# Kernel optimization log

Hardware: AMD Instinct MI355X
Metric: run time of the kernel (lower is better)

Reference implementation:

```python
import jax, jax.numpy as jnp
import numpy as np

D_MODEL = 1024
HEADS = 16
D_KEY = D_MODEL // HEADS


def setup_inputs() -> dict:
    key = jax.random.key(0)
    ks = jax.random.split(key, 7)
    B, S = 4, 2048
    queries = jax.random.normal(ks[0], (B, S, D_MODEL), dtype=jnp.float32)
    keys = jax.random.normal(ks[1], (B, S, D_MODEL), dtype=jnp.float32)
    values = jax.random.normal(ks[2], (B, S, D_MODEL), dtype=jnp.float32)
    scale = 1.0 / np.sqrt(D_MODEL)
    # Per-head projection weights, torch Linear layout [out=d_key, in=d_model], stacked over heads
    Wq = jax.random.uniform(ks[3], (HEADS, D_KEY, D_MODEL), jnp.float32, -scale, scale)
    Wk = jax.random.uniform(ks[4], (HEADS, D_KEY, D_MODEL), jnp.float32, -scale, scale)
    Wv = jax.random.uniform(ks[5], (HEADS, D_KEY, D_MODEL), jnp.float32, -scale, scale)
    Wo = jax.random.uniform(ks[6], (D_MODEL, D_MODEL), jnp.float32, -scale, scale)
    return {"queries": queries, "keys": keys, "values": values,
            "Wq": Wq, "Wk": Wk, "Wv": Wv, "Wo": Wo}


def reference(queries, keys, values, Wq, Wk, Wv, Wo):
    # Project per head: [B,S,D] x [H,K,D] -> [B,H,S,K]
    q = jnp.einsum('bsd,hkd->bhsk', queries, Wq)
    k = jnp.einsum('bsd,hkd->bhsk', keys, Wk)
    v = jnp.einsum('bsd,hkd->bhsk', values, Wv)
    attn = jnp.einsum('bhqk,bhsk->bhqs', q, k) / jnp.sqrt(jnp.float32(D_KEY))
    attn = jax.nn.softmax(attn, axis=-1)
    out = jnp.einsum('bhqs,bhsk->bhqk', attn, v)  # [B,H,S,K]
    B, H, S, K = out.shape
    # concat heads along last dim (head order = torch cat order)
    out = out.transpose(0, 2, 1, 3).reshape(B, S, H * K)
    return out @ Wo.T
```

## Files before the change

kernel.cpp:

```cpp
#include <hip/hip_runtime.h>
#include <hip/hip_bf16.h>

typedef __attribute__((ext_vector_type(8))) short short8;
typedef __attribute__((ext_vector_type(4))) short short4v;
typedef __attribute__((ext_vector_type(4))) float f32x4;
typedef __bf16 bf16x8 __attribute__((ext_vector_type(8)));
typedef __attribute__((ext_vector_type(2))) unsigned int u32x2;
typedef __attribute__((ext_vector_type(4))) unsigned int u32x4;

#define DEVI static __device__ __forceinline__

DEVI short f2bs(float f) {
    union { __hip_bfloat16 h; short s; } u;
    u.h = __float2bfloat16(f);
    return u.s;
}

DEVI unsigned pack2(float a, float b) {
    union { short s[2]; unsigned u; } u;
    u.s[0] = f2bs(a);
    u.s[1] = f2bs(b);
    return u.u;
}

DEVI void xchg(unsigned& x, unsigned& y) {
#if __has_builtin(__builtin_amdgcn_permlane32_swap) && __has_builtin(__builtin_amdgcn_permlane16_swap)
    u32x2 t = __builtin_amdgcn_permlane32_swap(x, y, false, false);
    u32x2 r = __builtin_amdgcn_permlane16_swap(t[0], t[1], false, false);
    x = r[0];
    y = r[1];
#else
    asm("v_permlane32_swap_b32 %0, %1" : "+v"(x), "+v"(y));
    asm("v_permlane16_swap_b32 %0, %1" : "+v"(x), "+v"(y));
#endif
}

DEVI f32x4 mfma16(short8 a, short8 b, f32x4 c) {
    return __builtin_amdgcn_mfma_f32_16x16x32_bf16(
        __builtin_bit_cast(bf16x8, a), __builtin_bit_cast(bf16x8, b), c, 0, 0, 0);
}

DEVI void glds16(const short* g, short* l) {
    __builtin_amdgcn_global_load_lds((const __attribute__((address_space(1))) void*)g,
                                     (__attribute__((address_space(3))) void*)l, 16, 0, 0);
}

__global__ __launch_bounds__(256) void cvt_all(const float4* __restrict__ q,
                                               const float4* __restrict__ k,
                                               const float4* __restrict__ v,
                                               const float4* __restrict__ wq,
                                               const float4* __restrict__ wk,
                                               const float4* __restrict__ wv,
                                               const float4* __restrict__ wo,
                                               short4v* __restrict__ dq,
                                               short4v* __restrict__ dk,
                                               short4v* __restrict__ dv,
                                               short4v* __restrict__ dwq,
                                               short4v* __restrict__ dwk,
                                               short4v* __restrict__ dwv,
                                               short4v* __restrict__ dwo) {
    int bid = blockIdx.x;
    float4 x;
    short4v s;
    if (bid < 8192) {
        int i = bid * 256 + threadIdx.x;
        x = q[i]; s.x = f2bs(x.x); s.y = f2bs(x.y); s.z = f2bs(x.z); s.w = f2bs(x.w); dq[i] = s;
        x = k[i]; s.x = f2bs(x.x); s.y = f2bs(x.y); s.z = f2bs(x.z); s.w = f2bs(x.w); dk[i] = s;
        x = v[i]; s.x = f2bs(x.x); s.y = f2bs(x.y); s.z = f2bs(x.z); s.w = f2bs(x.w); dv[i] = s;
    } else {
        int i = (bid - 8192) * 256 + threadIdx.x;
        x = wq[i]; s.x = f2bs(x.x); s.y = f2bs(x.y); s.z = f2bs(x.z); s.w = f2bs(x.w); dwq[i] = s;
        x = wk[i]; s.x = f2bs(x.x); s.y = f2bs(x.y); s.z = f2bs(x.z); s.w = f2bs(x.w); dwk[i] = s;
        x = wv[i]; s.x = f2bs(x.x); s.y = f2bs(x.y); s.z = f2bs(x.z); s.w = f2bs(x.w); dwv[i] = s;
        x = wo[i]; s.x = f2bs(x.x); s.y = f2bs(x.y); s.z = f2bs(x.z); s.w = f2bs(x.w); dwo[i] = s;
    }
}

template <typename EpiT>
DEVI void gemm_body(const short* A, const short* Bw, short* smem, int m0, int n0, EpiT epi) {
    const int t = threadIdx.x;
    const int lane = t & 63, w = t >> 6;
    const int col = lane & 15, quad = lane >> 4;
    const int wm = (w & 1) * 64, wn = (w >> 1) * 64;

    const short* pA0;
    const short* pA1;
    const short* pB0;
    const short* pB1;
    {
        int i0 = w * 64 + lane, i1 = (4 + w) * 64 + lane;
        int L0 = i0 >> 3, cc0 = (i0 & 7) ^ (L0 & 7);
        int r0 = 2 * L0 + (cc0 & 1), c0 = cc0 >> 1;
        int L1 = i1 >> 3, cc1 = (i1 & 7) ^ (L1 & 7);
        int r1 = 2 * L1 + (cc1 & 1), c1 = cc1 >> 1;
        pA0 = A + (size_t)(m0 + r0) * 1024 + c0 * 8;
        pA1 = A + (size_t)(m0 + r1) * 1024 + c1 * 8;
        pB0 = Bw + (size_t)(n0 + r0) * 1024 + c0 * 8;
        pB1 = Bw + (size_t)(n0 + r1) * 1024 + c1 * 8;
    }
    const int posa = (2 * quad + (col & 1)) ^ (col >> 1);
    const int base_a = wm * 32 + (col >> 1) * 64 + posa * 8;
    const int base_b = wn * 32 + (col >> 1) * 64 + posa * 8;

    f32x4 acc[4][4];
#pragma unroll
    for (int i = 0; i < 4; ++i)
#pragma unroll
        for (int j = 0; j < 4; ++j) acc[i][j] = (f32x4){0.f, 0.f, 0.f, 0.f};

    glds16(pA0, smem + w * 512);
    glds16(pA1, smem + (4 + w) * 512);
    glds16(pB0, smem + 4096 + w * 512);
    glds16(pB1, smem + 4096 + (4 + w) * 512);
    pA0 += 32; pA1 += 32; pB0 += 32; pB1 += 32;
    __syncthreads();

#pragma unroll 2
    for (int kt = 0; kt < 32; ++kt) {
        const int cur = kt & 1;
        const short* Cb = smem + cur * 8192;
        if (kt < 31) {
            short* Nb = smem + (cur ^ 1) * 8192;
            glds16(pA0, Nb + w * 512);
            glds16(pA1, Nb + (4 + w) * 512);
            glds16(pB0, Nb + 4096 + w * 512);
            glds16(pB1, Nb + 4096 + (4 + w) * 512);
            pA0 += 32; pA1 += 32; pB0 += 32; pB1 += 32;
        }
        short8 a[4], b[4];
#pragma unroll
        for (int i = 0; i < 4; ++i) a[i] = *(const short8*)(Cb + base_a + i * 512);
#pragma unroll
        for (int i = 0; i < 4; ++i) b[i] = *(const short8*)(Cb + 4096 + base_b + i * 512);
        __builtin_amdgcn_s_setprio(1);
#pragma unroll
        for (int mi = 0; mi < 4; ++mi)
#pragma unroll
            for (int ni = 0; ni < 4; ++ni)
                acc[mi][ni] = mfma16(a[mi], b[ni], acc[mi][ni]);
        __builtin_amdgcn_s_setprio(0);
        __syncthreads();
    }
    epi(acc, wm, wn, col, quad);
}

__global__ __launch_bounds__(256) void qkv_gemm(const short* __restrict__ xq,
                                                const short* __restrict__ xk,
                                                const short* __restrict__ xv,
                                                const short* __restrict__ wq,
                                                const short* __restrict__ wk,
                                                const short* __restrict__ wv,
                                                short* __restrict__ qp,
                                                short* __restrict__ kp,
                                                short* __restrict__ vpt, float qscale) {
    __shared__ __align__(16) short smem[17408];
    const int lin = blockIdx.x + (blockIdx.y << 3) + (blockIdx.z << 9);
    const int wgid = (lin & 7) * 192 + (lin >> 3);
    const int n0 = (wgid & 7) * 128;
    const int m0 = ((wgid >> 3) & 63) * 128;
    const int z = wgid >> 9;
    const short* A = (z == 0) ? xq : (z == 1) ? xk : xv;
    const short* W = (z == 0) ? wq : (z == 1) ? wk : wv;

    if (z < 2) {
        short* outs = (z == 0) ? qp : kp;
        const float scale = (z == 0) ? qscale : 1.0f;
        gemm_body(A, W, smem, m0, n0, [&](f32x4 (&acc)[4][4], int wm, int wn, int col, int quad) {
            short* T = smem;
#pragma unroll
            for (int mi = 0; mi < 4; ++mi)
#pragma unroll
                for (int ni = 0; ni < 4; ++ni)
#pragma unroll
                    for (int r = 0; r < 4; ++r)
                        T[(wm + mi * 16 + quad * 4 + r) * 136 + wn + ni * 16 + col] =
                            f2bs(acc[mi][ni][r] * scale);
            __syncthreads();
            int t = threadIdx.x;
            int ml = t >> 1, nh = (t & 1) * 64;
            int m = m0 + ml;
            int b = m >> 11, s = m & 2047;
#pragma unroll
            for (int j = 0; j < 8; ++j) {
                int n = n0 + nh + j * 8;
                short8 vv = *(const short8*)(T + ml * 136 + nh + j * 8);
                size_t off = ((size_t)(b * 16 + (n >> 6)) * 2048 + s) * 64 + (n & 63);
                *(short8*)(outs + off) = vv;
            }
        });
    } else {
        gemm_body(A, W, smem, m0, n0, [&](f32x4 (&acc)[4][4], int wm, int wn, int col, int quad) {
            short* T = smem;
#pragma unroll
            for (int mi = 0; mi < 4; ++mi)
#pragma unroll
                for (int ni = 0; ni < 4; ++ni) {
                    int n_l = wn + ni * 16 + col;
                    int m_l = wm + mi * 16 + quad * 4;
                    short4v sv;
                    sv.x = f2bs(acc[mi][ni][0]); sv.y = f2bs(acc[mi][ni][1]);
                    sv.z = f2bs(acc[mi][ni][2]); sv.w = f2bs(acc[mi][ni][3]);
                    *(short4v*)(T + n_l * 132 + m_l) = sv;
                }
            __syncthreads();
            int t = threadIdx.x;
            int nrow = t >> 1, mh = (t & 1) * 64;
            int b = m0 >> 11, s0 = m0 & 2047;
            size_t base = ((size_t)(b * 1024 + n0 + nrow)) * 2048 + s0 + mh;
#pragma unroll
            for (int j = 0; j < 16; ++j) {
                unsigned long long vv = *(const unsigned long long*)(T + nrow * 132 + mh + j * 4);
                *(unsigned long long*)(vpt + base + j * 4) = vv;
            }
        });
    }
}

__global__ __launch_bounds__(256) void out_gemm(const short* __restrict__ ao,
                                                const short* __restrict__ wo,
                                                float* __restrict__ outf) {
    __shared__ __align__(16) short smem[16896];
    const int lin = blockIdx.x + (blockIdx.y << 3);
    const int wgid = (lin & 7) * 64 + (lin >> 3);
    const int n0 = (wgid & 7) * 128;
    const int m0 = (wgid >> 3) * 128;
    gemm_body(ao, wo, smem, m0, n0, [&](f32x4 (&acc)[4][4], int wm, int wn, int col, int quad) {
#pragma unroll
        for (int mi = 0; mi < 4; ++mi)
#pragma unroll
            for (int ni = 0; ni < 4; ++ni)
#pragma unroll
                for (int r = 0; r < 4; ++r) {
                    int m = m0 + wm + mi * 16 + quad * 4 + r;
                    int n = n0 + wn + ni * 16 + col;
                    outf[(size_t)m * 1024 + n] = acc[mi][ni][r];
                }
    });
}

__global__ __launch_bounds__(256, 4) void flash_attn(const short* __restrict__ qp,
                                                     const short* __restrict__ kp,
                                                     const short* __restrict__ vpt,
                                                     short* __restrict__ ao) {
    __shared__ __align__(16) short smem[16384];
    short* Ks2 = smem;
    short* Vs2 = smem + 8192;

    const int t = threadIdx.x, lane = t & 63, w = t >> 6;
    const int col = lane & 15, quad = lane >> 4;
    const int bh = blockIdx.x, q0 = blockIdx.y * 128;
    const short* qb = qp + (size_t)bh * 2048 * 64;
    const short* kb = kp + (size_t)bh * 2048 * 64;
    const short* vb = vpt + (size_t)bh * 64 * 2048;

#pragma unroll
    for (int j = 0; j < 4; ++j) {
        int cbase = (j * 4 + w) * 64;
        int c = cbase + lane;
        int row = c >> 3, kc = (c & 7) ^ (row & 7);
        glds16(qb + (size_t)(q0 + row) * 64 + kc * 8, smem + cbase * 8);
    }
    __syncthreads();
    short8 bQ[2][2];
#pragma unroll
    for (int qi = 0; qi < 2; ++qi)
#pragma unroll
        for (int ks = 0; ks < 2; ++ks) {
            int row = w * 32 + qi * 16 + col;
            int kc = (ks * 4 + quad) ^ (col & 7);
            bQ[qi][ks] = *(const short8*)(smem + (row * 8 + kc) * 8);
        }
    __syncthreads();

    const int base2_0 = col * 64 + ((quad ^ (col & 7)) * 8);
    const int base2_1 = col * 64 + (((4 + quad) ^ (col & 7)) * 8);

    const short* kg0;
    const short* kg1;
    const short* vg0;
    const short* vg1;
    {
        int c0 = w * 64 + lane, c1 = (4 + w) * 64 + lane;
        int r0 = c0 >> 3, p0 = c0 & 7, r1 = c1 >> 3, p1 = c1 & 7;
        kg0 = kb + r0 * 64 + ((p0 ^ (r0 & 7)) * 8);
        kg1 = kb + r1 * 64 + ((p1 ^ (r1 & 7)) * 8);
        vg0 = vb + (size_t)r0 * 2048 + ((p0 ^ (r0 & 7)) * 8);
        vg1 = vb + (size_t)r1 * 2048 + ((p1 ^ (r1 & 7)) * 8);
    }

    f32x4 acc_o[2][4], acc_l[2];
#pragma unroll
    for (int qi = 0; qi < 2; ++qi) {
        acc_l[qi] = (f32x4){0.f, 0.f, 0.f, 0.f};
#pragma unroll
        for (int ni = 0; ni < 4; ++ni) acc_o[qi][ni] = (f32x4){0.f, 0.f, 0.f, 0.f};
    }
    const short ONE = 0x3F80;
    const short8 vones = {ONE, ONE, ONE, ONE, ONE, ONE, ONE, ONE};

    glds16(kg0, Ks2 + w * 512);
    glds16(kg1, Ks2 + (4 + w) * 512);
    glds16(vg0, Vs2 + w * 512);
    glds16(vg1, Vs2 + (4 + w) * 512);
    kg0 += 4096; kg1 += 4096; vg0 += 64; vg1 += 64;
    __syncthreads();

#pragma unroll 2
    for (int kt = 0; kt < 32; ++kt) {
        const int cur = kt & 1;
        if (kt < 31) {
            const int nxt = cur ^ 1;
            glds16(kg0, Ks2 + nxt * 4096 + w * 512);
            glds16(kg1, Ks2 + nxt * 4096 + (4 + w) * 512);
            glds16(vg0, Vs2 + nxt * 4096 + w * 512);
            glds16(vg1, Vs2 + nxt * 4096 + (4 + w) * 512);
            kg0 += 4096; kg1 += 4096; vg0 += 64; vg1 += 64;
        }
        const short* Ks = Ks2 + cur * 4096;
        const short* Vs = Vs2 + cur * 4096;

#pragma unroll
        for (int g = 0; g < 2; ++g) {
            unsigned pdw[2][4];
#pragma unroll
            for (int h = 0; h < 2; ++h) {
                const int kei = g * 2 + h;
                f32x4 st0 = (f32x4){0.f, 0.f, 0.f, 0.f};
                f32x4 st1 = (f32x4){0.f, 0.f, 0.f, 0.f};
                __builtin_amdgcn_s_setprio(1);
                {
                    short8 aK0 = *(const short8*)(Ks + base2_0 + kei * 1024);
                    st0 = mfma16(aK0, bQ[0][0], st0);
                    st1 = mfma16(aK0, bQ[1][0], st1);
                    short8 aK1 = *(const short8*)(Ks + base2_1 + kei * 1024);
                    st0 = mfma16(aK1, bQ[0][1], st0);
                    st1 = mfma16(aK1, bQ[1][1], st1);
                }
                __builtin_amdgcn_s_setprio(0);
                {
                    float p0 = __builtin_amdgcn_exp2f(st0[0]);
                    float p1 = __builtin_amdgcn_exp2f(st0[1]);
                    float p2 = __builtin_amdgcn_exp2f(st0[2]);
                    float p3 = __builtin_amdgcn_exp2f(st0[3]);
                    pdw[0][h * 2] = pack2(p0, p1);
                    pdw[0][h * 2 + 1] = pack2(p2, p3);
                }
                {
                    float p0 = __builtin_amdgcn_exp2f(st1[0]);
                    float p1 = __builtin_amdgcn_exp2f(st1[1]);
                    float p2 = __builtin_amdgcn_exp2f(st1[2]);
                    float p3 = __builtin_amdgcn_exp2f(st1[3]);
                    pdw[1][h * 2] = pack2(p0, p1);
                    pdw[1][h * 2 + 1] = pack2(p2, p3);
                }
            }
            xchg(pdw[0][0], pdw[0][2]);
            xchg(pdw[0][1], pdw[0][3]);
            xchg(pdw[1][0], pdw[1][2]);
            xchg(pdw[1][1], pdw[1][3]);
            u32x4 pv0 = {pdw[0][0], pdw[0][1], pdw[0][2], pdw[0][3]};
            u32x4 pv1 = {pdw[1][0], pdw[1][1], pdw[1][2], pdw[1][3]};
            short8 pa0 = __builtin_bit_cast(short8, pv0);
            short8 pa1 = __builtin_bit_cast(short8, pv1);

            const int vb2 = (g == 0) ? base2_0 : base2_1;
            __builtin_amdgcn_s_setprio(1);
#pragma unroll
            for (int ni = 0; ni < 4; ++ni) {
                short8 bv = *(const short8*)(Vs + vb2 + ni * 1024);
                acc_o[0][ni] = mfma16(pa0, bv, acc_o[0][ni]);
                acc_o[1][ni] = mfma16(pa1, bv, acc_o[1][ni]);
            }
            acc_l[0] = mfma16(pa0, vones, acc_l[0]);
            acc_l[1] = mfma16(pa1, vones, acc_l[1]);
            __builtin_amdgcn_s_setprio(0);
        }
        __syncthreads();
    }

    const int b = bh >> 4, hd = bh & 15;
#pragma unroll
    for (int qi = 0; qi < 2; ++qi)
#pragma unroll
        for (int r = 0; r < 4; ++r) {
            float inv = 1.0f / acc_l[qi][r];
            int q = q0 + w * 32 + qi * 16 + quad * 4 + r;
#pragma unroll
            for (int ni = 0; ni < 4; ++ni)
                ao[((size_t)(b * 2048 + q)) * 1024 + hd * 64 + ni * 16 + col] =
                    f2bs(acc_o[qi][ni][r] * inv);
        }
}

extern "C" void kernel_launch(void* const* d_in, const int* in_sizes, int n_in,
                              void* d_out, int out_size, void* d_ws, size_t ws_size,
                              hipStream_t stream) {
    const float* q  = (const float*)d_in[0];
    const float* k  = (const float*)d_in[1];
    const float* v  = (const float*)d_in[2];
    const float* Wq = (const float*)d_in[3];
    const float* Wk = (const float*)d_in[4];
    const float* Wv = (const float*)d_in[5];
    const float* Wo = (const float*)d_in[6];
    float* out = (float*)d_out;

    short* ws = (short*)d_ws;
    const size_t SZ = (size_t)64 * 2048 * 64;
    const size_t WZ = (size_t)1024 * 1024;
    short* xq  = ws;
    short* xk  = ws + SZ;
    short* xv  = ws + 2 * SZ;
    short* qp  = ws + 3 * SZ;
    short* kp  = ws + 4 * SZ;
    short* wqb = ws + 5 * SZ;
    short* wkb = wqb + WZ;
    short* wvb = wqb + 2 * WZ;
    short* wob = wqb + 3 * WZ;
    short* ao  = xq;
    short* vpt = (short*)d_out;

    const float QSCALE = 0.125f * 1.44269504088896f;

    cvt_all<<<dim3(9216), dim3(256), 0, stream>>>(
        (const float4*)q, (const float4*)k, (const float4*)v, (const float4*)Wq,
        (const float4*)Wk, (const float4*)Wv, (const float4*)Wo, (short4v*)xq, (short4v*)xk,
        (short4v*)xv, (short4v*)wqb, (short4v*)wkb, (short4v*)wvb, (short4v*)wob);
    dim3 blk(256);
    qkv_gemm<<<dim3(8, 64, 3), blk, 0, stream>>>(xq, xk, xv, wqb, wkb, wvb, qp, kp, vpt, QSCALE);
    flash_attn<<<dim3(64, 16), blk, 0, stream>>>(qp, kp, vpt, ao);
    out_gemm<<<dim3(8, 64), blk, 0, stream>>>(ao, wob, out);
}
```

Measured before the change: 331.0 us.

## Switch flash attention inner loop to 32x32x16 bf16 MFMA tiles

Rewrites the attention kernel's QK^T and PV products to use 32x32x16 MFMA instead of 16x16x32, with each wave owning a 32-row Q tile. The P fragment shuffle drops to a single permlane32 swap and the row-sum accumulator becomes one 16-wide tile. The aim is fewer MFMA issues, fewer LDS fragment reads and fewer lane permutes per key tile. In exchange it changes the register layout and exp/pack scheduling, with some risk to register pressure and occupancy at four waves per SIMD.

```diff
diff --git a/kernel.cpp b/kernel.cpp
--- a/kernel.cpp
+++ b/kernel.cpp
@@ -4,6 +4,7 @@
 typedef __attribute__((ext_vector_type(8))) short short8;
 typedef __attribute__((ext_vector_type(4))) short short4v;
 typedef __attribute__((ext_vector_type(4))) float f32x4;
+typedef __attribute__((ext_vector_type(16))) float f32x16;
 typedef __bf16 bf16x8 __attribute__((ext_vector_type(8)));
 typedef __attribute__((ext_vector_type(2))) unsigned int u32x2;
 typedef __attribute__((ext_vector_type(4))) unsigned int u32x4;
@@ -23,20 +24,17 @@
     return u.u;
 }
 
-DEVI void xchg(unsigned& x, unsigned& y) {
-#if __has_builtin(__builtin_amdgcn_permlane32_swap) && __has_builtin(__builtin_amdgcn_permlane16_swap)
-    u32x2 t = __builtin_amdgcn_permlane32_swap(x, y, false, false);
-    u32x2 r = __builtin_amdgcn_permlane16_swap(t[0], t[1], false, false);
-    x = r[0];
-    y = r[1];
-#else
-    asm("v_permlane32_swap_b32 %0, %1" : "+v"(x), "+v"(y));
-    asm("v_permlane16_swap_b32 %0, %1" : "+v"(x), "+v"(y));
-#endif
+DEVI u32x2 pl32(unsigned x, unsigned y) {
+    return __builtin_amdgcn_permlane32_swap(x, y, false, false);
 }
 
 DEVI f32x4 mfma16(short8 a, short8 b, f32x4 c) {
     return __builtin_amdgcn_mfma_f32_16x16x32_bf16(
+        __builtin_bit_cast(bf16x8, a), __builtin_bit_cast(bf16x8, b), c, 0, 0, 0);
+}
+
+DEVI f32x16 mfma32(short8 a, short8 b, f32x16 c) {
+    return __builtin_amdgcn_mfma_f32_32x32x16_bf16(
         __builtin_bit_cast(bf16x8, a), __builtin_bit_cast(bf16x8, b), c, 0, 0, 0);
 }
 
@@ -247,7 +245,7 @@
     short* Vs2 = smem + 8192;
 
     const int t = threadIdx.x, lane = t & 63, w = t >> 6;
-    const int col = lane & 15, quad = lane >> 4;
+    const int rl = lane & 31, hi = lane >> 5;
     const int bh = blockIdx.x, q0 = blockIdx.y * 128;
     const short* qb = qp + (size_t)bh * 2048 * 64;
     const short* kb = kp + (size_t)bh * 2048 * 64;
@@ -261,19 +259,16 @@
         glds16(qb + (size_t)(q0 + row) * 64 + kc * 8, smem + cbase * 8);
     }
     __syncthreads();
-    short8 bQ[2][2];
-#pragma unroll
-    for (int qi = 0; qi < 2; ++qi)
-#pragma unroll
-        for (int ks = 0; ks < 2; ++ks) {
-            int row = w * 32 + qi * 16 + col;
-            int kc = (ks * 4 + quad) ^ (col & 7);
-            bQ[qi][ks] = *(const short8*)(smem + (row * 8 + kc) * 8);
-        }
+
+    int offA[4];
+#pragma unroll
+    for (int j = 0; j < 4; ++j) offA[j] = (((j * 2 + hi) ^ (rl & 7)) * 8) + rl * 64;
+
+    short8 bQ0 = *(const short8*)(smem + w * 2048 + offA[0]);
+    short8 bQ1 = *(const short8*)(smem + w * 2048 + offA[1]);
+    short8 bQ2 = *(const short8*)(smem + w * 2048 + offA[2]);
+    short8 bQ3 = *(const short8*)(smem + w * 2048 + offA[3]);
     __syncthreads();
-
-    const int base2_0 = col * 64 + ((quad ^ (col & 7)) * 8);
-    const int base2_1 = col * 64 + (((4 + quad) ^ (col & 7)) * 8);
 
     const short* kg0;
     const short* kg1;
@@ -288,13 +283,9 @@
         vg1 = vb + (size_t)r1 * 2048 + ((p1 ^ (r1 & 7)) * 8);
     }
 
-    f32x4 acc_o[2][4], acc_l[2];
-#pragma unroll
-    for (int qi = 0; qi < 2; ++qi) {
-        acc_l[qi] = (f32x4){0.f, 0.f, 0.f, 0.f};
-#pragma unroll
-        for (int ni = 0; ni < 4; ++ni) acc_o[qi][ni] = (f32x4){0.f, 0.f, 0.f, 0.f};
-    }
+    const f32x16 kZ = {0.f, 0.f, 0.f, 0.f, 0.f, 0.f, 0.f, 0.f,
+                       0.f, 0.f, 0.f, 0.f, 0.f, 0.f, 0.f, 0.f};
+    f32x16 acc_o0 = kZ, acc_o1 = kZ, acc_l = kZ;
     const short ONE = 0x3F80;
     const short8 vones = {ONE, ONE, ONE, ONE, ONE, ONE, ONE, ONE};
 
@@ -321,58 +312,48 @@
 
 #pragma unroll
         for (int g = 0; g < 2; ++g) {
-            unsigned pdw[2][4];
-#pragma unroll
-            for (int h = 0; h < 2; ++h) {
-                const int kei = g * 2 + h;
-                f32x4 st0 = (f32x4){0.f, 0.f, 0.f, 0.f};
-                f32x4 st1 = (f32x4){0.f, 0.f, 0.f, 0.f};
-                __builtin_amdgcn_s_setprio(1);
-                {
-                    short8 aK0 = *(const short8*)(Ks + base2_0 + kei * 1024);
-                    st0 = mfma16(aK0, bQ[0][0], st0);
-                    st1 = mfma16(aK0, bQ[1][0], st1);
-                    short8 aK1 = *(const short8*)(Ks + base2_1 + kei * 1024);
-                    st0 = mfma16(aK1, bQ[0][1], st0);
-                    st1 = mfma16(aK1, bQ[1][1], st1);
-                }
-                __builtin_amdgcn_s_setprio(0);
-                {
-                    float p0 = __builtin_amdgcn_exp2f(st0[0]);
-                    float p1 = __builtin_amdgcn_exp2f(st0[1]);
-                    float p2 = __builtin_amdgcn_exp2f(st0[2]);
-                    float p3 = __builtin_amdgcn_exp2f(st0[3]);
-                    pdw[0][h * 2] = pack2(p0, p1);
-                    pdw[0][h * 2 + 1] = pack2(p2, p3);
-                }
-                {
-                    float p0 = __builtin_amdgcn_exp2f(st1[0]);
-                    float p1 = __builtin_amdgcn_exp2f(st1[1]);
-                    float p2 = __builtin_amdgcn_exp2f(st1[2]);
-                    float p3 = __builtin_amdgcn_exp2f(st1[3]);
-                    pdw[1][h * 2] = pack2(p0, p1);
-                    pdw[1][h * 2 + 1] = pack2(p2, p3);
-                }
-            }
-            xchg(pdw[0][0], pdw[0][2]);
-            xchg(pdw[0][1], pdw[0][3]);
-            xchg(pdw[1][0], pdw[1][2]);
-            xchg(pdw[1][1], pdw[1][3]);
-            u32x4 pv0 = {pdw[0][0], pdw[0][1], pdw[0][2], pdw[0][3]};
-            u32x4 pv1 = {pdw[1][0], pdw[1][1], pdw[1][2], pdw[1][3]};
-            short8 pa0 = __builtin_bit_cast(short8, pv0);
-            short8 pa1 = __builtin_bit_cast(short8, pv1);
-
-            const int vb2 = (g == 0) ? base2_0 : base2_1;
+            const short* Kg = Ks + g * 2048;
             __builtin_amdgcn_s_setprio(1);
-#pragma unroll
-            for (int ni = 0; ni < 4; ++ni) {
-                short8 bv = *(const short8*)(Vs + vb2 + ni * 1024);
-                acc_o[0][ni] = mfma16(pa0, bv, acc_o[0][ni]);
-                acc_o[1][ni] = mfma16(pa1, bv, acc_o[1][ni]);
-            }
-            acc_l[0] = mfma16(pa0, vones, acc_l[0]);
-            acc_l[1] = mfma16(pa1, vones, acc_l[1]);
+            short8 a0 = *(const short8*)(Kg + offA[0]);
+            f32x16 st = mfma32(a0, bQ0, kZ);
+            short8 a1k = *(const short8*)(Kg + offA[1]);
+            st = mfma32(a1k, bQ1, st);
+            short8 a2k = *(const short8*)(Kg + offA[2]);
+            st = mfma32(a2k, bQ2, st);
+            short8 a3k = *(const short8*)(Kg + offA[3]);
+            st = mfma32(a3k, bQ3, st);
+            __builtin_amdgcn_s_setprio(0);
+
+            unsigned d0 = pack2(__builtin_amdgcn_exp2f(st[0]), __builtin_amdgcn_exp2f(st[1]));
+            unsigned d1 = pack2(__builtin_amdgcn_exp2f(st[2]), __builtin_amdgcn_exp2f(st[3]));
+            unsigned d2 = pack2(__builtin_amdgcn_exp2f(st[4]), __builtin_amdgcn_exp2f(st[5]));
+            unsigned d3 = pack2(__builtin_amdgcn_exp2f(st[6]), __builtin_amdgcn_exp2f(st[7]));
+            u32x2 t02 = pl32(d0, d2);
+            u32x2 t13 = pl32(d1, d3);
+            u32x4 a1v = {t02[0], t13[0], t02[1], t13[1]};
+            short8 pA1 = __builtin_bit_cast(short8, a1v);
+            __builtin_amdgcn_s_setprio(1);
+            short8 bv00 = *(const short8*)(Vs + offA[g * 2]);
+            acc_o0 = mfma32(pA1, bv00, acc_o0);
+            short8 bv01 = *(const short8*)(Vs + 2048 + offA[g * 2]);
+            acc_o1 = mfma32(pA1, bv01, acc_o1);
+            acc_l = mfma32(pA1, vones, acc_l);
+            __builtin_amdgcn_s_setprio(0);
+
+            unsigned d4 = pack2(__builtin_amdgcn_exp2f(st[8]), __builtin_amdgcn_exp2f(st[9]));
+            unsigned d5 = pack2(__builtin_amdgcn_exp2f(st[10]), __builtin_amdgcn_exp2f(st[11]));
+            unsigned d6 = pack2(__builtin_amdgcn_exp2f(st[12]), __builtin_amdgcn_exp2f(st[13]));
+            unsigned d7 = pack2(__builtin_amdgcn_exp2f(st[14]), __builtin_amdgcn_exp2f(st[15]));
+            u32x2 t46 = pl32(d4, d6);
+            u32x2 t57 = pl32(d5, d7);
+            u32x4 a2v = {t46[0], t57[0], t46[1], t57[1]};
+            short8 pA2 = __builtin_bit_cast(short8, a2v);
+            __builtin_amdgcn_s_setprio(1);
+            short8 bv10 = *(const short8*)(Vs + offA[g * 2 + 1]);
+            acc_o0 = mfma32(pA2, bv10, acc_o0);
+            short8 bv11 = *(const short8*)(Vs + 2048 + offA[g * 2 + 1]);
+            acc_o1 = mfma32(pA2, bv11, acc_o1);
+            acc_l = mfma32(pA2, vones, acc_l);
             __builtin_amdgcn_s_setprio(0);
         }
         __syncthreads();
@@ -380,16 +361,13 @@
 
     const int b = bh >> 4, hd = bh & 15;
 #pragma unroll
-    for (int qi = 0; qi < 2; ++qi)
-#pragma unroll
-        for (int r = 0; r < 4; ++r) {
-            float inv = 1.0f / acc_l[qi][r];
-            int q = q0 + w * 32 + qi * 16 + quad * 4 + r;
-#pragma unroll
-            for (int ni = 0; ni < 4; ++ni)
-                ao[((size_t)(b * 2048 + q)) * 1024 + hd * 64 + ni * 16 + col] =
-                    f2bs(acc_o[qi][ni][r] * inv);
-        }
+    for (int r = 0; r < 16; ++r) {
+        float inv = 1.0f / acc_l[r];
+        int qrow = q0 + w * 32 + (r & 3) + 8 * (r >> 2) + 4 * hi;
+        size_t base = ((size_t)(b * 2048 + qrow)) * 1024 + hd * 64 + rl;
+        ao[base] = f2bs(acc_o0[r] * inv);
+        ao[base + 32] = f2bs(acc_o1[r] * inv);
+    }
 }
 
 extern "C" void kernel_launch(void* const* d_in, const int* in_sizes, int n_in,
```

After: 341.0 us. 3.0% more time.

## Fuse fp32-to-bf16 activation conversion into QKV GEMM A-tile loading

Applied to the files above, without the earlier changes.

Removes the separate conversion pass over the query, key and value activations. The QKV projection GEMM now loads fp32 A tiles through registers, packs them to bf16 and stores them into shared memory, while only the weights are still converted up front. This avoids writing and re-reading the bf16 activation copies. The cost is double-size fp32 A reads repeated across column blocks and register-path loads in place of direct-to-LDS loads, which adds register pressure and load latency.

```diff
diff --git a/kernel.cpp b/kernel.cpp
--- a/kernel.cpp
+++ b/kernel.cpp
@@ -45,35 +45,21 @@
                                      (__attribute__((address_space(3))) void*)l, 16, 0, 0);
 }
 
-__global__ __launch_bounds__(256) void cvt_all(const float4* __restrict__ q,
-                                               const float4* __restrict__ k,
-                                               const float4* __restrict__ v,
-                                               const float4* __restrict__ wq,
-                                               const float4* __restrict__ wk,
-                                               const float4* __restrict__ wv,
-                                               const float4* __restrict__ wo,
-                                               short4v* __restrict__ dq,
-                                               short4v* __restrict__ dk,
-                                               short4v* __restrict__ dv,
-                                               short4v* __restrict__ dwq,
-                                               short4v* __restrict__ dwk,
-                                               short4v* __restrict__ dwv,
-                                               short4v* __restrict__ dwo) {
-    int bid = blockIdx.x;
+__global__ __launch_bounds__(256) void cvt_w(const float4* __restrict__ wq,
+                                             const float4* __restrict__ wk,
+                                             const float4* __restrict__ wv,
+                                             const float4* __restrict__ wo,
+                                             short4v* __restrict__ dwq,
+                                             short4v* __restrict__ dwk,
+                                             short4v* __restrict__ dwv,
+                                             short4v* __restrict__ dwo) {
+    int i = blockIdx.x * 256 + threadIdx.x;
     float4 x;
     short4v s;
-    if (bid < 8192) {
-        int i = bid * 256 + threadIdx.x;
-        x = q[i]; s.x = f2bs(x.x); s.y = f2bs(x.y); s.z = f2bs(x.z); s.w = f2bs(x.w); dq[i] = s;
-        x = k[i]; s.x = f2bs(x.x); s.y = f2bs(x.y); s.z = f2bs(x.z); s.w = f2bs(x.w); dk[i] = s;
-        x = v[i]; s.x = f2bs(x.x); s.y = f2bs(x.y); s.z = f2bs(x.z); s.w = f2bs(x.w); dv[i] = s;
-    } else {
-        int i = (bid - 8192) * 256 + threadIdx.x;
-        x = wq[i]; s.x = f2bs(x.x); s.y = f2bs(x.y); s.z = f2bs(x.z); s.w = f2bs(x.w); dwq[i] = s;
-        x = wk[i]; s.x = f2bs(x.x); s.y = f2bs(x.y); s.z = f2bs(x.z); s.w = f2bs(x.w); dwk[i] = s;
-        x = wv[i]; s.x = f2bs(x.x); s.y = f2bs(x.y); s.z = f2bs(x.z); s.w = f2bs(x.w); dwv[i] = s;
-        x = wo[i]; s.x = f2bs(x.x); s.y = f2bs(x.y); s.z = f2bs(x.z); s.w = f2bs(x.w); dwo[i] = s;
-    }
+    x = wq[i]; s.x = f2bs(x.x); s.y = f2bs(x.y); s.z = f2bs(x.z); s.w = f2bs(x.w); dwq[i] = s;
+    x = wk[i]; s.x = f2bs(x.x); s.y = f2bs(x.y); s.z = f2bs(x.z); s.w = f2bs(x.w); dwk[i] = s;
+    x = wv[i]; s.x = f2bs(x.x); s.y = f2bs(x.y); s.z = f2bs(x.z); s.w = f2bs(x.w); dwv[i] = s;
+    x = wo[i]; s.x = f2bs(x.x); s.y = f2bs(x.y); s.z = f2bs(x.z); s.w = f2bs(x.w); dwo[i] = s;
 }
 
 template <typename EpiT>
@@ -144,9 +130,98 @@
     epi(acc, wm, wn, col, quad);
 }
 
-__global__ __launch_bounds__(256) void qkv_gemm(const short* __restrict__ xq,
-                                                const short* __restrict__ xk,
-                                                const short* __restrict__ xv,
+template <typename EpiT>
+DEVI void gemm_body_f32a(const float* A32, const short* Bw, short* smem, int m0, int n0,
+                         EpiT epi) {
+    const int t = threadIdx.x;
+    const int lane = t & 63, w = t >> 6;
+    const int col = lane & 15, quad = lane >> 4;
+    const int wm = (w & 1) * 64, wn = (w >> 1) * 64;
+
+    const float* pA0;
+    const float* pA1;
+    const short* pB0;
+    const short* pB1;
+    int d0, d1;
+    {
+        int i0 = w * 64 + lane, i1 = (4 + w) * 64 + lane;
+        int L0 = i0 >> 3, cc0 = (i0 & 7) ^ (L0 & 7);
+        int r0 = 2 * L0 + (cc0 & 1), c0 = cc0 >> 1;
+        int L1 = i1 >> 3, cc1 = (i1 & 7) ^ (L1 & 7);
+        int r1 = 2 * L1 + (cc1 & 1), c1 = cc1 >> 1;
+        pA0 = A32 + (size_t)(m0 + r0) * 1024 + c0 * 8;
+        pA1 = A32 + (size_t)(m0 + r1) * 1024 + c1 * 8;
+        pB0 = Bw + (size_t)(n0 + r0) * 1024 + c0 * 8;
+        pB1 = Bw + (size_t)(n0 + r1) * 1024 + c1 * 8;
+        d0 = i0 * 8;
+        d1 = i1 * 8;
+    }
+    const int posa = (2 * quad + (col & 1)) ^ (col >> 1);
+    const int base_a = wm * 32 + (col >> 1) * 64 + posa * 8;
+    const int base_b = wn * 32 + (col >> 1) * 64 + posa * 8;
+
+    f32x4 acc[4][4];
+#pragma unroll
+    for (int i = 0; i < 4; ++i)
+#pragma unroll
+        for (int j = 0; j < 4; ++j) acc[i][j] = (f32x4){0.f, 0.f, 0.f, 0.f};
+
+    {
+        float4 a00 = *(const float4*)pA0, a01 = *(const float4*)(pA0 + 4);
+        float4 a10 = *(const float4*)pA1, a11 = *(const float4*)(pA1 + 4);
+        glds16(pB0, smem + 4096 + w * 512);
+        glds16(pB1, smem + 4096 + (4 + w) * 512);
+        pA0 += 32; pA1 += 32; pB0 += 32; pB1 += 32;
+        u32x4 s0 = {pack2(a00.x, a00.y), pack2(a00.z, a00.w),
+                    pack2(a01.x, a01.y), pack2(a01.z, a01.w)};
+        u32x4 s1 = {pack2(a10.x, a10.y), pack2(a10.z, a10.w),
+                    pack2(a11.x, a11.y), pack2(a11.z, a11.w)};
+        *(u32x4*)(smem + d0) = s0;
+        *(u32x4*)(smem + d1) = s1;
+    }
+    __syncthreads();
+
+#pragma unroll 2
+    for (int kt = 0; kt < 32; ++kt) {
+        const int cur = kt & 1;
+        const short* Cb = smem + cur * 8192;
+        short* Nb = smem + (cur ^ 1) * 8192;
+        float4 a00, a01, a10, a11;
+        if (kt < 31) {
+            a00 = *(const float4*)pA0; a01 = *(const float4*)(pA0 + 4);
+            a10 = *(const float4*)pA1; a11 = *(const float4*)(pA1 + 4);
+            glds16(pB0, Nb + 4096 + w * 512);
+            glds16(pB1, Nb + 4096 + (4 + w) * 512);
+            pA0 += 32; pA1 += 32; pB0 += 32; pB1 += 32;
+        }
+        short8 a[4], b[4];
+#pragma unroll
+        for (int i = 0; i < 4; ++i) a[i] = *(const short8*)(Cb + base_a + i * 512);
+#pragma unroll
+        for (int i = 0; i < 4; ++i) b[i] = *(const short8*)(Cb + 4096 + base_b + i * 512);
+        __builtin_amdgcn_s_setprio(1);
+#pragma unroll
+        for (int mi = 0; mi < 4; ++mi)
+#pragma unroll
+            for (int ni = 0; ni < 4; ++ni)
+                acc[mi][ni] = mfma16(a[mi], b[ni], acc[mi][ni]);
+        __builtin_amdgcn_s_setprio(0);
+        if (kt < 31) {
+            u32x4 s0 = {pack2(a00.x, a00.y), pack2(a00.z, a00.w),
+                        pack2(a01.x, a01.y), pack2(a01.z, a01.w)};
+            u32x4 s1 = {pack2(a10.x, a10.y), pack2(a10.z, a10.w),
+                        pack2(a11.x, a11.y), pack2(a11.z, a11.w)};
+            *(u32x4*)(Nb + d0) = s0;
+            *(u32x4*)(Nb + d1) = s1;
+        }
+        __syncthreads();
+    }
+    epi(acc, wm, wn, col, quad);
+}
+
+__global__ __launch_bounds__(256) void qkv_gemm(const float* __restrict__ xq,
+                                                const float* __restrict__ xk,
+                                                const float* __restrict__ xv,
                                                 const short* __restrict__ wq,
                                                 const short* __restrict__ wk,
                                                 const short* __restrict__ wv,
@@ -159,13 +234,14 @@
     const int n0 = (wgid & 7) * 128;
     const int m0 = ((wgid >> 3) & 63) * 128;
     const int z = wgid >> 9;
-    const short* A = (z == 0) ? xq : (z == 1) ? xk : xv;
+    const float* A = (z == 0) ? xq : (z == 1) ? xk : xv;
     const short* W = (z == 0) ? wq : (z == 1) ? wk : wv;
 
     if (z < 2) {
         short* outs = (z == 0) ? qp : kp;
         const float scale = (z == 0) ? qscale : 1.0f;
-        gemm_body(A, W, smem, m0, n0, [&](f32x4 (&acc)[4][4], int wm, int wn, int col, int quad) {
+        gemm_body_f32a(A, W, smem, m0, n0,
+                       [&](f32x4 (&acc)[4][4], int wm, int wn, int col, int quad) {
             short* T = smem;
 #pragma unroll
             for (int mi = 0; mi < 4; ++mi)
@@ -189,7 +265,8 @@
             }
         });
     } else {
-        gemm_body(A, W, smem, m0, n0, [&](f32x4 (&acc)[4][4], int wm, int wn, int col, int quad) {
+        gemm_body_f32a(A, W, smem, m0, n0,
+                       [&](f32x4 (&acc)[4][4], int wm, int wn, int col, int quad) {
             short* T = smem;
 #pragma unroll
             for (int mi = 0; mi < 4; ++mi)
@@ -407,26 +484,22 @@
     short* ws = (short*)d_ws;
     const size_t SZ = (size_t)64 * 2048 * 64;
     const size_t WZ = (size_t)1024 * 1024;
-    short* xq  = ws;
-    short* xk  = ws + SZ;
-    short* xv  = ws + 2 * SZ;
-    short* qp  = ws + 3 * SZ;
-    short* kp  = ws + 4 * SZ;
-    short* wqb = ws + 5 * SZ;
+    short* ao  = ws;
+    short* qp  = ws + SZ;
+    short* kp  = ws + 2 * SZ;
+    short* wqb = ws + 3 * SZ;
     short* wkb = wqb + WZ;
     short* wvb = wqb + 2 * WZ;
     short* wob = wqb + 3 * WZ;
-    short* ao  = xq;
     short* vpt = (short*)d_out;
 
     const float QSCALE = 0.125f * 1.44269504088896f;
 
-    cvt_all<<<dim3(9216), dim3(256), 0, stream>>>(
-        (const float4*)q, (const float4*)k, (const float4*)v, (const float4*)Wq,
-        (const float4*)Wk, (const float4*)Wv, (const float4*)Wo, (short4v*)xq, (short4v*)xk,
-        (short4v*)xv, (short4v*)wqb, (short4v*)wkb, (short4v*)wvb, (short4v*)wob);
+    cvt_w<<<dim3(1024), dim3(256), 0, stream>>>(
+        (const float4*)Wq, (const float4*)Wk, (const float4*)Wv, (const float4*)Wo,
+        (short4v*)wqb, (short4v*)wkb, (short4v*)wvb, (short4v*)wob);
     dim3 blk(256);
-    qkv_gemm<<<dim3(8, 64, 3), blk, 0, stream>>>(xq, xk, xv, wqb, wkb, wvb, qp, kp, vpt, QSCALE);
+    qkv_gemm<<<dim3(8, 64, 3), blk, 0, stream>>>(q, k, v, wqb, wkb, wvb, qp, kp, vpt, QSCALE);
     flash_attn<<<dim3(64, 16), blk, 0, stream>>>(qp, kp, vpt, ao);
     out_gemm<<<dim3(8, 64), blk, 0, stream>>>(ao, wob, out);
 }
```

After: 370.9 us. 12.1% more time.
